# Optimization experiments

Measured on AMD Instinct MI355X. Metric: run time of the kernel, lower is better.

The kernel has to match this reference:

```python
import jax, jax.numpy as jnp
import numpy as np

N = 32768          # total points (32 clouds x 1024 points)
K = 32             # neighbors per point -> E = N*K edges
E = N * K
NHID = 128
NCLASS = 16
PTS = 1024         # points per cloud (hardcoded in forward's view)


def _lin_init(key, out_dim, in_dim):
    kw, kb = jax.random.split(key)
    w = jax.random.normal(kw, (out_dim, in_dim), jnp.float32) * (1.0 / np.sqrt(in_dim))
    b = jax.random.normal(kb, (out_dim,), jnp.float32) * 0.01
    return w, b


def setup_inputs() -> dict:
    key = jax.random.key(0)
    ks = jax.random.split(key, 12)
    pos = jax.random.normal(ks[0], (N, 3), jnp.float32)
    edge_index = jax.random.randint(ks[1], (2, E), 0, N, dtype=jnp.int64)
    h = NHID
    enc1_w, enc1_b = _lin_init(ks[2], h // 2, 3)
    enc2_w, enc2_b = _lin_init(ks[3], h // 2, h // 2)
    enc3_w, enc3_b = _lin_init(ks[4], h, h // 2)
    loc_w, loc_b = _lin_init(ks[5], 2 * h, h + 3)   # local_nn: [x_j, pos_j - pos_i]
    glob_w, glob_b = _lin_init(ks[6], 3 * h, 2 * h)  # global_nn
    dec1_w, dec1_b = _lin_init(ks[7], 2 * h, 3 * h)
    dec2_w, dec2_b = _lin_init(ks[8], h, 2 * h)
    dec3_w, dec3_b = _lin_init(ks[9], NCLASS, h)
    return dict(pos=pos, edge_index=edge_index,
                enc1_w=enc1_w, enc1_b=enc1_b, enc2_w=enc2_w, enc2_b=enc2_b,
                enc3_w=enc3_w, enc3_b=enc3_b, loc_w=loc_w, loc_b=loc_b,
                glob_w=glob_w, glob_b=glob_b, dec1_w=dec1_w, dec1_b=dec1_b,
                dec2_w=dec2_w, dec2_b=dec2_b, dec3_w=dec3_w, dec3_b=dec3_b)


def _lin(x, w, b):
    return x @ w.T + b


def reference(pos, edge_index,
              enc1_w, enc1_b, enc2_w, enc2_b, enc3_w, enc3_b,
              loc_w, loc_b, glob_w, glob_b,
              dec1_w, dec1_b, dec2_w, dec2_b, dec3_w, dec3_b):
    # encoder MLP on raw xyz
    x = jnp.tanh(_lin(pos, enc1_w, enc1_b))
    x = jnp.tanh(_lin(x, enc2_w, enc2_b))
    x = jnp.tanh(_lin(x, enc3_w, enc3_b))          # [N, NHID]

    # PointNetConv (PyG default add_self_loops=True)
    loop = jnp.arange(N, dtype=edge_index.dtype)
    src = jnp.concatenate([edge_index[0], loop])   # j (neighbor / source)
    dst = jnp.concatenate([edge_index[1], loop])   # i (center / target)
    rel = pos[src] - pos[dst]                      # [E+N, 3]
    msg = jnp.concatenate([x[src], rel], axis=1)   # [E+N, NHID+3]
    msg = _lin(msg, loc_w, loc_b)                  # local_nn -> [E+N, 2*NHID]
    summed = jax.ops.segment_sum(msg, dst, num_segments=N)
    cnt = jax.ops.segment_sum(jnp.ones((msg.shape[0],), msg.dtype), dst,
                              num_segments=N)
    agg = summed / jnp.maximum(cnt, 1.0)[:, None]  # scatter-mean
    x = _lin(agg, glob_w, glob_b)                  # global_nn -> [N, 3*NHID]

    # per-cloud mean pool then decoder MLP
    x = x.reshape(N // PTS, PTS, -1).mean(axis=1)  # [B, 3*NHID]
    x = jnp.tanh(_lin(x, dec1_w, dec1_b))
    x = jnp.tanh(_lin(x, dec2_w, dec2_b))
    x = _lin(x, dec3_w, dec3_b)                    # [B, NCLASS]
    return x
```

## Files before the change

kernel.cpp:

```cpp
#include <hip/hip_runtime.h>
#include <hip/hip_bf16.h>

#define NPTS   32768
#define EEDGES 1048576
#define PTSC   1024
#define NCLOUD 32
#define ADIM   132
#define MROW   (NCLOUD * ADIM)
#define NBLK   256
#define CHUNK  (NPTS / NBLK)
#define FXSCALE 16777216.0f

__global__ __launch_bounds__(256) void prep_kernel(
    const float* __restrict__ w2, const float* __restrict__ w3,
    const float* __restrict__ locw, const float* __restrict__ globw,
    const float* __restrict__ d1w, const float* __restrict__ d2w,
    const float* __restrict__ d3w,
    float* __restrict__ w2T, float* __restrict__ w3T,
    float* __restrict__ locT, float* __restrict__ globT,
    float* __restrict__ d1T, float* __restrict__ d2T, float* __restrict__ d3T,
    int* __restrict__ cnt) {
  int idx = blockIdx.x * 256 + threadIdx.x;
  if (idx >= 277248) {
    cnt[idx - 277248] = 0;
    return;
  }
  const float* src; float* dst; int R, C;
  if (idx < 4096)        { src = w2;   dst = w2T;   R = 64;  C = 64;  }
  else if (idx < 12288)  { src = w3;   dst = w3T;   R = 128; C = 64;  idx -= 4096; }
  else if (idx < 45824)  { src = locw; dst = locT;  R = 256; C = 131; idx -= 12288; }
  else if (idx < 144128) { src = globw;dst = globT; R = 384; C = 256; idx -= 45824; }
  else if (idx < 242432) { src = d1w;  dst = d1T;   R = 256; C = 384; idx -= 144128; }
  else if (idx < 275200) { src = d2w;  dst = d2T;   R = 128; C = 256; idx -= 242432; }
  else                   { src = d3w;  dst = d3T;   R = 16;  C = 128; idx -= 275200; }
  int c = idx / R, r = idx % R;
  dst[idx] = src[r * C + c];
}

__device__ __forceinline__ unsigned pack_bf16(float a, float b) {
  __hip_bfloat162 o;
  o.x = __float2bfloat16(a);
  o.y = __float2bfloat16(b);
  return *reinterpret_cast<unsigned*>(&o);
}

__device__ __forceinline__ float rlane(float x, int k) {
  return __int_as_float(__builtin_amdgcn_readlane(__float_as_int(x), k));
}

__device__ __forceinline__ float fast_tanh(float x) {
  float e = __expf(2.0f * x);
  return 1.0f - 2.0f * __builtin_amdgcn_rcpf(e + 1.0f);
}

__global__ __launch_bounds__(256) void hist_kernel(const int* __restrict__ ei,
                                                   int* __restrict__ cnt) {
  int t = blockIdx.x * 256 + threadIdx.x;
  const int4* d4 = reinterpret_cast<const int4*>(ei + EEDGES);
  int4 v = d4[t];
  atomicAdd(&cnt[v.x], 1);
  atomicAdd(&cnt[v.y], 1);
  atomicAdd(&cnt[v.z], 1);
  atomicAdd(&cnt[v.w], 1);
}

__global__ __launch_bounds__(256) void invwi_kernel(const int* __restrict__ cnt,
                                                    int* __restrict__ invwi,
                                                    int* __restrict__ ai) {
  int i = blockIdx.x * 256 + threadIdx.x;
  int v = (int)rintf(FXSCALE / (float)(cnt[i] + 1));
  invwi[i] = v;
  int4 z = make_int4(0, 0, 0, 0);
  int4* row = reinterpret_cast<int4*>(ai + i * 32);
#pragma unroll
  for (int q = 0; q < 8; ++q) row[q] = z;
  ai[i * 32 + (i >> 10)] = v;
}

__global__ __launch_bounds__(256) void enc_ascatter_kernel(
    const int* __restrict__ ei, const int* __restrict__ invwi, int* __restrict__ ai,
    const float* __restrict__ pos,
    const float* __restrict__ w1, const float* __restrict__ b1,
    const float* __restrict__ w2T, const float* __restrict__ b2,
    const float* __restrict__ w3T, const float* __restrict__ b3,
    __hip_bfloat16* __restrict__ xb) {
  if (blockIdx.x < EEDGES / 1024) {
    int t = blockIdx.x * 256 + threadIdx.x;
    const int4* s4 = reinterpret_cast<const int4*>(ei);
    const int4* d4 = reinterpret_cast<const int4*>(ei + EEDGES);
    int4 s = s4[t];
    int4 d = d4[t];
    int w0 = invwi[d.x];
    int w1i = invwi[d.y];
    int w2i = invwi[d.z];
    int w3i = invwi[d.w];
    atomicAdd(&ai[s.x * 32 + (d.x >> 10)], w0);
    atomicAdd(&ai[s.y * 32 + (d.y >> 10)], w1i);
    atomicAdd(&ai[s.z * 32 + (d.z >> 10)], w2i);
    atomicAdd(&ai[s.w * 32 + (d.w >> 10)], w3i);
    return;
  }
  int wid  = ((blockIdx.x - EEDGES / 1024) * 256 + threadIdx.x) >> 6;
  int lane = threadIdx.x & 63;
  int i0 = __builtin_amdgcn_readfirstlane(wid * 8);

  float w1a = w1[lane * 3 + 0], w1b = w1[lane * 3 + 1], w1c = w1[lane * 3 + 2];
  float bb1 = b1[lane];

  float h1[8];
#pragma unroll
  for (int p = 0; p < 8; ++p) {
    int i = i0 + p;
    float px = pos[i * 3 + 0], py = pos[i * 3 + 1], pz = pos[i * 3 + 2];
    h1[p] = fast_tanh(w1a * px + w1b * py + w1c * pz + bb1);
  }

  float bb2 = b2[lane];
  float acc2[8];
#pragma unroll
  for (int p = 0; p < 8; ++p) acc2[p] = bb2;
#pragma unroll
  for (int k = 0; k < 64; ++k) {
    float w = w2T[k * 64 + lane];
#pragma unroll
    for (int p = 0; p < 8; ++p) acc2[p] += w * rlane(h1[p], k);
  }
  float h2[8];
#pragma unroll
  for (int p = 0; p < 8; ++p) h2[p] = fast_tanh(acc2[p]);

  int r0 = 2 * lane;
  float bb3a = b3[r0], bb3b = b3[r0 + 1];
  float acc3a[8], acc3b[8];
#pragma unroll
  for (int p = 0; p < 8; ++p) { acc3a[p] = bb3a; acc3b[p] = bb3b; }
#pragma unroll
  for (int k = 0; k < 64; ++k) {
    float2 w = *reinterpret_cast<const float2*>(w3T + k * 128 + r0);
#pragma unroll
    for (int p = 0; p < 8; ++p) {
      float h = rlane(h2[p], k);
      acc3a[p] += w.x * h;
      acc3b[p] += w.y * h;
    }
  }
#pragma unroll
  for (int p = 0; p < 8; ++p) {
    int i = i0 + p;
    unsigned o = pack_bf16(fast_tanh(acc3a[p]), fast_tanh(acc3b[p]));
    *reinterpret_cast<unsigned*>(xb + (size_t)i * 128 + r0) = o;
  }
}

__global__ __launch_bounds__(256) void contract_kernel(
    const ushort* __restrict__ xu, const float* __restrict__ pos,
    const int* __restrict__ ai, float* __restrict__ partial) {
  int w = threadIdx.x >> 6, l = threadIdx.x & 63;
  int cw = w * 8;
  int s0 = blockIdx.x * CHUNK;
  int s1 = s0 + CHUNK;

  float a0[8] = {0,0,0,0,0,0,0,0};
  float a1[8] = {0,0,0,0,0,0,0,0};
  float a2[8] = {0,0,0,0,0,0,0,0};

#pragma unroll 2
  for (int s = s0; s < s1; ++s) {
    unsigned xr = *reinterpret_cast<const unsigned*>(xu + (size_t)s * 128 + 2 * l);
    float f0 = __uint_as_float(xr << 16);
    float f1 = __uint_as_float(xr & 0xffff0000u);
    float p  = (l < 3) ? pos[s * 3 + l] : 0.f;
    const int4* ar = reinterpret_cast<const int4*>(ai + (size_t)s * 32 + cw);
    int4 A0 = ar[0], A1 = ar[1];
    float af[8] = {(float)A0.x, (float)A0.y, (float)A0.z, (float)A0.w,
                   (float)A1.x, (float)A1.y, (float)A1.z, (float)A1.w};
#pragma unroll
    for (int cc = 0; cc < 8; ++cc) {
      a0[cc] += af[cc] * f0;
      a1[cc] += af[cc] * f1;
      a2[cc] += af[cc] * p;
    }
  }

  const float SC = 1.0f / FXSCALE;
  float* pb = partial + (size_t)blockIdx.x * MROW;
#pragma unroll
  for (int cc = 0; cc < 8; ++cc) {
    pb[(cw + cc) * ADIM + 2 * l]     = a0[cc] * SC;
    pb[(cw + cc) * ADIM + 2 * l + 1] = a1[cc] * SC;
    if (l < 3) pb[(cw + cc) * ADIM + 128 + l] = a2[cc] * SC;
  }
}

__global__ __launch_bounds__(1024) void final_kernel(
    const float* __restrict__ partial, const float* __restrict__ pos,
    const float* __restrict__ locT, const float* __restrict__ loc_b,
    const float* __restrict__ globT, const float* __restrict__ glob_b,
    const float* __restrict__ d1T, const float* __restrict__ d1b,
    const float* __restrict__ d2T, const float* __restrict__ d2b,
    const float* __restrict__ d3T, const float* __restrict__ d3b,
    float* __restrict__ out) {
  int c = blockIdx.x, t = threadIdx.x;
  int wv = t >> 6, ln = t & 63;

  __shared__ float sw[16][3];
  __shared__ float possum[3];
  __shared__ float r4[544];
  __shared__ float msh[144];
  __shared__ float ttsh[256];
  __shared__ float ush[384];
  __shared__ float ash[256];
  __shared__ float bvsh[128];
  __shared__ float ptl2[4352];

  {
    const float* pr = pos + ((size_t)c * PTSC + t) * 3;
    float s0 = pr[0], s1 = pr[1], s2 = pr[2];
#pragma unroll
    for (int m_ = 32; m_ > 0; m_ >>= 1) {
      s0 += __shfl_xor(s0, m_);
      s1 += __shfl_xor(s1, m_);
      s2 += __shfl_xor(s2, m_);
    }
    if (ln == 0) { sw[wv][0] = s0; sw[wv][1] = s1; sw[wv][2] = s2; }
  }
  {
    int dd = t >> 2, qq = t & 3;
    if (dd < 132) {
      float s = 0.f;
      int b0 = qq * 64;
      const float* pp = partial + c * ADIM + dd;
      for (int bk = b0; bk < b0 + 64; ++bk)
        s += pp[(size_t)bk * MROW];
      r4[dd * 4 + qq] = s;
    }
  }
  __syncthreads();
  if (t < 48) {
    int d = t >> 4, idx = t & 15;
    float v = sw[idx][d];
#pragma unroll
    for (int m_ = 8; m_ > 0; m_ >>= 1) v += __shfl_xor(v, m_);
    if (idx == 0) possum[d] = v;
  }
  __syncthreads();

  if (t < 144) {
    if (t < 128) {
      float s = (r4[4 * t] + r4[4 * t + 1]) + (r4[4 * t + 2] + r4[4 * t + 3]);
      msh[t] = s * (1.0f / (float)PTSC);
    } else if (t < 131) {
      float s = (r4[4 * t] + r4[4 * t + 1]) + (r4[4 * t + 2] + r4[4 * t + 3]);
      msh[t] = (s - possum[t - 128]) * (1.0f / (float)PTSC);
    } else {
      msh[t] = 0.f;
    }
  }
  __syncthreads();

  {
    int p = wv, og = ln;
    float4 wvv[9];
#pragma unroll
    for (int j = 0; j < 9; ++j) {
      int k = p * 9 + j;
      wvv[j] = *reinterpret_cast<const float4*>(locT + (size_t)k * 256 + og * 4);
    }
    float a0, a1, a2, a3;
    if (p == 0) {
      float4 b = *reinterpret_cast<const float4*>(loc_b + og * 4);
      a0 = b.x; a1 = b.y; a2 = b.z; a3 = b.w;
    } else { a0 = a1 = a2 = a3 = 0.f; }
#pragma unroll
    for (int j = 0; j < 9; ++j) {
      float x = msh[p * 9 + j];
      a0 += wvv[j].x * x; a1 += wvv[j].y * x; a2 += wvv[j].z * x; a3 += wvv[j].w * x;
    }
    ptl2[(p * 4 + 0) * 66 + og] = a0;
    ptl2[(p * 4 + 1) * 66 + og] = a1;
    ptl2[(p * 4 + 2) * 66 + og] = a2;
    ptl2[(p * 4 + 3) * 66 + og] = a3;
  }
  __syncthreads();
  if (t < 256) {
    int og = t >> 2, sub = t & 3;
    float s = 0.f;
#pragma unroll
    for (int p = 0; p < 16; ++p) s += ptl2[(p * 4 + sub) * 66 + og];
    ttsh[t] = s;
  }
  __syncthreads();

  if (t < 768) {
    int p = t / 96, og = t - p * 96;
    float a0, a1, a2, a3;
    if (p == 0) {
      float4 b = *reinterpret_cast<const float4*>(glob_b + og * 4);
      a0 = b.x; a1 = b.y; a2 = b.z; a3 = b.w;
    } else { a0 = a1 = a2 = a3 = 0.f; }
#pragma unroll
    for (int B = 0; B < 4; ++B) {
      float4 wvv[8];
#pragma unroll
      for (int j = 0; j < 8; ++j) {
        int k = p * 32 + B * 8 + j;
        wvv[j] = *reinterpret_cast<const float4*>(globT + (size_t)k * 384 + og * 4);
      }
#pragma unroll
      for (int j = 0; j < 8; ++j) {
        float x = ttsh[p * 32 + B * 8 + j];
        a0 += wvv[j].x * x; a1 += wvv[j].y * x; a2 += wvv[j].z * x; a3 += wvv[j].w * x;
      }
    }
    ptl2[(p * 4 + 0) * 98 + og] = a0;
    ptl2[(p * 4 + 1) * 98 + og] = a1;
    ptl2[(p * 4 + 2) * 98 + og] = a2;
    ptl2[(p * 4 + 3) * 98 + og] = a3;
  }
  __syncthreads();
  if (t < 384) {
    int og = t >> 2, sub = t & 3;
    float s = 0.f;
#pragma unroll
    for (int p = 0; p < 8; ++p) s += ptl2[(p * 4 + sub) * 98 + og];
    ush[t] = s;
  }
  __syncthreads();

  {
    int p = wv, og = ln;
    float a0, a1, a2, a3;
    if (p == 0) {
      float4 b = *reinterpret_cast<const float4*>(d1b + og * 4);
      a0 = b.x; a1 = b.y; a2 = b.z; a3 = b.w;
    } else { a0 = a1 = a2 = a3 = 0.f; }
#pragma unroll
    for (int B = 0; B < 3; ++B) {
      float4 wvv[8];
#pragma unroll
      for (int j = 0; j < 8; ++j) {
        int k = p * 24 + B * 8 + j;
        wvv[j] = *reinterpret_cast<const float4*>(d1T + (size_t)k * 256 + og * 4);
      }
#pragma unroll
      for (int j = 0; j < 8; ++j) {
        float x = ush[p * 24 + B * 8 + j];
        a0 += wvv[j].x * x; a1 += wvv[j].y * x; a2 += wvv[j].z * x; a3 += wvv[j].w * x;
      }
    }
    ptl2[(p * 4 + 0) * 66 + og] = a0;
    ptl2[(p * 4 + 1) * 66 + og] = a1;
    ptl2[(p * 4 + 2) * 66 + og] = a2;
    ptl2[(p * 4 + 3) * 66 + og] = a3;
  }
  __syncthreads();
  if (t < 256) {
    int og = t >> 2, sub = t & 3;
    float s = 0.f;
#pragma unroll
    for (int p = 0; p < 16; ++p) s += ptl2[(p * 4 + sub) * 66 + og];
    ash[t] = tanhf(s);
  }
  __syncthreads();

  {
    int p = t >> 5, og = t & 31;
    float4 wvv[8];
#pragma unroll
    for (int j = 0; j < 8; ++j) {
      int k = p * 8 + j;
      wvv[j] = *reinterpret_cast<const float4*>(d2T + (size_t)k * 128 + og * 4);
    }
    float a0, a1, a2, a3;
    if (p == 0) {
      float4 b = *reinterpret_cast<const float4*>(d2b + og * 4);
      a0 = b.x; a1 = b.y; a2 = b.z; a3 = b.w;
    } else { a0 = a1 = a2 = a3 = 0.f; }
#pragma unroll
    for (int j = 0; j < 8; ++j) {
      float x = ash[p * 8 + j];
      a0 += wvv[j].x * x; a1 += wvv[j].y * x; a2 += wvv[j].z * x; a3 += wvv[j].w * x;
    }
    ptl2[(p * 4 + 0) * 34 + og] = a0;
    ptl2[(p * 4 + 1) * 34 + og] = a1;
    ptl2[(p * 4 + 2) * 34 + og] = a2;
    ptl2[(p * 4 + 3) * 34 + og] = a3;
  }
  __syncthreads();
  if (t < 128) {
    int og = t >> 2, sub = t & 3;
    float s = 0.f;
#pragma unroll
    for (int p = 0; p < 32; ++p) s += ptl2[(p * 4 + sub) * 34 + og];
    bvsh[t] = tanhf(s);
  }
  __syncthreads();

  {
    int o = wv, k = ln;
    if (o < 16) {
      float acc = d3T[k * 16 + o] * bvsh[k] + d3T[(k + 64) * 16 + o] * bvsh[k + 64];
#pragma unroll
      for (int m_ = 32; m_ > 0; m_ >>= 1) acc += __shfl_xor(acc, m_);
      if (ln == 0) out[c * 16 + o] = acc + d3b[o];
    }
  }
}

extern "C" void kernel_launch(void* const* d_in, const int* in_sizes, int n_in,
                              void* d_out, int out_size, void* d_ws, size_t ws_size,
                              hipStream_t stream) {
  const float* pos    = (const float*)d_in[0];
  const int*   ei     = (const int*)d_in[1];
  const float* enc1_w = (const float*)d_in[2];
  const float* enc1_b = (const float*)d_in[3];
  const float* enc2_w = (const float*)d_in[4];
  const float* enc2_b = (const float*)d_in[5];
  const float* enc3_w = (const float*)d_in[6];
  const float* enc3_b = (const float*)d_in[7];
  const float* loc_w  = (const float*)d_in[8];
  const float* loc_b  = (const float*)d_in[9];
  const float* glob_w = (const float*)d_in[10];
  const float* glob_b = (const float*)d_in[11];
  const float* d1w    = (const float*)d_in[12];
  const float* d1b    = (const float*)d_in[13];
  const float* d2w    = (const float*)d_in[14];
  const float* d2b    = (const float*)d_in[15];
  const float* d3w    = (const float*)d_in[16];
  const float* d3b    = (const float*)d_in[17];
  float* out = (float*)d_out;

  char* ws = (char*)d_ws;
  size_t o = 0;
  __hip_bfloat16* xb = (__hip_bfloat16*)(ws + o); o += 8388608;
  int*   ai    = (int*)  (ws + o); o += 4194304;
  int*   cnt   = (int*)  (ws + o); o += 131072;
  int*   invwi = (int*)  (ws + o); o += 131072;
  float* Macc  = (float*)(ws + o); o += 17408;
  float* w2T   = (float*)(ws + o); o += 16384;
  float* w3T   = (float*)(ws + o); o += 32768;
  float* locT  = (float*)(ws + o); o += 134144;
  float* globT = (float*)(ws + o); o += 393216;
  float* d1T   = (float*)(ws + o); o += 393216;
  float* d2T   = (float*)(ws + o); o += 131072;
  float* d3T   = (float*)(ws + o); o += 8192;
  float* partial = (float*)(ws + o);
  (void)ws_size;
  (void)Macc;

  prep_kernel<<<1211, 256, 0, stream>>>(enc2_w, enc3_w, loc_w, glob_w, d1w, d2w, d3w,
                                        w2T, w3T, locT, globT, d1T, d2T, d3T, cnt);
  hist_kernel<<<EEDGES / 1024, 256, 0, stream>>>(ei, cnt);
  invwi_kernel<<<NPTS / 256, 256, 0, stream>>>(cnt, invwi, ai);
  enc_ascatter_kernel<<<EEDGES / 1024 + NPTS / 32, 256, 0, stream>>>(
      ei, invwi, ai, pos, enc1_w, enc1_b, w2T, enc2_b, w3T, enc3_b, xb);
  contract_kernel<<<NBLK, 256, 0, stream>>>((const ushort*)xb, pos, ai, partial);
  final_kernel<<<NCLOUD, 1024, 0, stream>>>(partial, pos, locT, loc_b, globT, glob_b,
                                            d1T, d1b, d2T, d2b, d3T, d3b, out);
}
```

Measured before the change: 170.3 us.

## Fuse degree histogram with encoder and drop inverse-weight kernel

Moves the zeroing of the adjacency-weight buffer into the prep kernel and runs the degree histogram in the same launch as the encoder MLP. The inverse-degree weights are now computed on the fly from the counts inside the scatter and contract kernels, and the self-loop term is added in contract instead of being written to memory. This removes one launch and the invwi buffer. In exchange the scatter runs as a separate launch after the encoder rather than overlapping with it, and the weight is recomputed per edge.

```diff
diff --git a/kernel.cpp b/kernel.cpp
--- a/kernel.cpp
+++ b/kernel.cpp
@@ -19,8 +19,12 @@
     float* __restrict__ w2T, float* __restrict__ w3T,
     float* __restrict__ locT, float* __restrict__ globT,
     float* __restrict__ d1T, float* __restrict__ d2T, float* __restrict__ d3T,
-    int* __restrict__ cnt) {
+    int* __restrict__ cnt, int* __restrict__ ai) {
   int idx = blockIdx.x * 256 + threadIdx.x;
+  if (idx >= 310016) {
+    reinterpret_cast<int4*>(ai)[idx - 310016] = make_int4(0, 0, 0, 0);
+    return;
+  }
   if (idx >= 277248) {
     cnt[idx - 277248] = 0;
     return;
@@ -53,32 +57,12 @@
   return 1.0f - 2.0f * __builtin_amdgcn_rcpf(e + 1.0f);
 }
 
-__global__ __launch_bounds__(256) void hist_kernel(const int* __restrict__ ei,
-                                                   int* __restrict__ cnt) {
-  int t = blockIdx.x * 256 + threadIdx.x;
-  const int4* d4 = reinterpret_cast<const int4*>(ei + EEDGES);
-  int4 v = d4[t];
-  atomicAdd(&cnt[v.x], 1);
-  atomicAdd(&cnt[v.y], 1);
-  atomicAdd(&cnt[v.z], 1);
-  atomicAdd(&cnt[v.w], 1);
-}
-
-__global__ __launch_bounds__(256) void invwi_kernel(const int* __restrict__ cnt,
-                                                    int* __restrict__ invwi,
-                                                    int* __restrict__ ai) {
-  int i = blockIdx.x * 256 + threadIdx.x;
-  int v = (int)rintf(FXSCALE / (float)(cnt[i] + 1));
-  invwi[i] = v;
-  int4 z = make_int4(0, 0, 0, 0);
-  int4* row = reinterpret_cast<int4*>(ai + i * 32);
-#pragma unroll
-  for (int q = 0; q < 8; ++q) row[q] = z;
-  ai[i * 32 + (i >> 10)] = v;
-}
-
-__global__ __launch_bounds__(256) void enc_ascatter_kernel(
-    const int* __restrict__ ei, const int* __restrict__ invwi, int* __restrict__ ai,
+__device__ __forceinline__ int invw_fx(int deg) {
+  return (int)rintf(FXSCALE / (float)(deg + 1));
+}
+
+__global__ __launch_bounds__(256) void hist_enc_kernel(
+    const int* __restrict__ ei, int* __restrict__ cnt,
     const float* __restrict__ pos,
     const float* __restrict__ w1, const float* __restrict__ b1,
     const float* __restrict__ w2T, const float* __restrict__ b2,
@@ -86,18 +70,12 @@
     __hip_bfloat16* __restrict__ xb) {
   if (blockIdx.x < EEDGES / 1024) {
     int t = blockIdx.x * 256 + threadIdx.x;
-    const int4* s4 = reinterpret_cast<const int4*>(ei);
     const int4* d4 = reinterpret_cast<const int4*>(ei + EEDGES);
-    int4 s = s4[t];
-    int4 d = d4[t];
-    int w0 = invwi[d.x];
-    int w1i = invwi[d.y];
-    int w2i = invwi[d.z];
-    int w3i = invwi[d.w];
-    atomicAdd(&ai[s.x * 32 + (d.x >> 10)], w0);
-    atomicAdd(&ai[s.y * 32 + (d.y >> 10)], w1i);
-    atomicAdd(&ai[s.z * 32 + (d.z >> 10)], w2i);
-    atomicAdd(&ai[s.w * 32 + (d.w >> 10)], w3i);
+    int4 v = d4[t];
+    atomicAdd(&cnt[v.x], 1);
+    atomicAdd(&cnt[v.y], 1);
+    atomicAdd(&cnt[v.z], 1);
+    atomicAdd(&cnt[v.w], 1);
     return;
   }
   int wid  = ((blockIdx.x - EEDGES / 1024) * 256 + threadIdx.x) >> 6;
@@ -152,9 +130,28 @@
   }
 }
 
+__global__ __launch_bounds__(256) void ascatter_kernel(const int* __restrict__ ei,
+                                                       const int* __restrict__ cnt,
+                                                       int* __restrict__ ai) {
+  int t = blockIdx.x * 256 + threadIdx.x;
+  const int4* s4 = reinterpret_cast<const int4*>(ei);
+  const int4* d4 = reinterpret_cast<const int4*>(ei + EEDGES);
+  int4 s = s4[t];
+  int4 d = d4[t];
+  int c0 = cnt[d.x];
+  int c1 = cnt[d.y];
+  int c2 = cnt[d.z];
+  int c3 = cnt[d.w];
+  atomicAdd(&ai[s.x * 32 + (d.x >> 10)], invw_fx(c0));
+  atomicAdd(&ai[s.y * 32 + (d.y >> 10)], invw_fx(c1));
+  atomicAdd(&ai[s.z * 32 + (d.z >> 10)], invw_fx(c2));
+  atomicAdd(&ai[s.w * 32 + (d.w >> 10)], invw_fx(c3));
+}
+
 __global__ __launch_bounds__(256) void contract_kernel(
     const ushort* __restrict__ xu, const float* __restrict__ pos,
-    const int* __restrict__ ai, float* __restrict__ partial) {
+    const int* __restrict__ ai, const int* __restrict__ cnt,
+    float* __restrict__ partial) {
   int w = threadIdx.x >> 6, l = threadIdx.x & 63;
   int cw = w * 8;
   int s0 = blockIdx.x * CHUNK;
@@ -172,8 +169,11 @@
     float p  = (l < 3) ? pos[s * 3 + l] : 0.f;
     const int4* ar = reinterpret_cast<const int4*>(ai + (size_t)s * 32 + cw);
     int4 A0 = ar[0], A1 = ar[1];
-    float af[8] = {(float)A0.x, (float)A0.y, (float)A0.z, (float)A0.w,
-                   (float)A1.x, (float)A1.y, (float)A1.z, (float)A1.w};
+    int Ai[8] = {A0.x, A0.y, A0.z, A0.w, A1.x, A1.y, A1.z, A1.w};
+    int cd = (s >> 10) - cw;
+    if (cd >= 0 && cd < 8) Ai[cd] += invw_fx(cnt[s]);
+    float af[8] = {(float)Ai[0], (float)Ai[1], (float)Ai[2], (float)Ai[3],
+                   (float)Ai[4], (float)Ai[5], (float)Ai[6], (float)Ai[7]};
 #pragma unroll
     for (int cc = 0; cc < 8; ++cc) {
       a0[cc] += af[cc] * f0;
@@ -435,8 +435,6 @@
   __hip_bfloat16* xb = (__hip_bfloat16*)(ws + o); o += 8388608;
   int*   ai    = (int*)  (ws + o); o += 4194304;
   int*   cnt   = (int*)  (ws + o); o += 131072;
-  int*   invwi = (int*)  (ws + o); o += 131072;
-  float* Macc  = (float*)(ws + o); o += 17408;
   float* w2T   = (float*)(ws + o); o += 16384;
   float* w3T   = (float*)(ws + o); o += 32768;
   float* locT  = (float*)(ws + o); o += 134144;
@@ -446,15 +444,13 @@
   float* d3T   = (float*)(ws + o); o += 8192;
   float* partial = (float*)(ws + o);
   (void)ws_size;
-  (void)Macc;
-
-  prep_kernel<<<1211, 256, 0, stream>>>(enc2_w, enc3_w, loc_w, glob_w, d1w, d2w, d3w,
-                                        w2T, w3T, locT, globT, d1T, d2T, d3T, cnt);
-  hist_kernel<<<EEDGES / 1024, 256, 0, stream>>>(ei, cnt);
-  invwi_kernel<<<NPTS / 256, 256, 0, stream>>>(cnt, invwi, ai);
-  enc_ascatter_kernel<<<EEDGES / 1024 + NPTS / 32, 256, 0, stream>>>(
-      ei, invwi, ai, pos, enc1_w, enc1_b, w2T, enc2_b, w3T, enc3_b, xb);
-  contract_kernel<<<NBLK, 256, 0, stream>>>((const ushort*)xb, pos, ai, partial);
+
+  prep_kernel<<<2235, 256, 0, stream>>>(enc2_w, enc3_w, loc_w, glob_w, d1w, d2w, d3w,
+                                        w2T, w3T, locT, globT, d1T, d2T, d3T, cnt, ai);
+  hist_enc_kernel<<<EEDGES / 1024 + NPTS / 32, 256, 0, stream>>>(
+      ei, cnt, pos, enc1_w, enc1_b, w2T, enc2_b, w3T, enc3_b, xb);
+  ascatter_kernel<<<EEDGES / 1024, 256, 0, stream>>>(ei, cnt, ai);
+  contract_kernel<<<NBLK, 256, 0, stream>>>((const ushort*)xb, pos, ai, cnt, partial);
   final_kernel<<<NCLOUD, 1024, 0, stream>>>(partial, pos, locT, loc_b, globT, glob_b,
                                             d1T, d1b, d2T, d2b, d3T, d3b, out);
 }
```

Result: slower. 181.2 us (+6.4%).
